# Performance work log

Hardware: AMD Instinct MI355X
Metric: run time of the kernel (lower is better)

The kernel has to match this reference:

```python
import jax, jax.numpy as jnp
import numpy as np

ATT = 256
NUM_GENES = 2128
HIDDEN = 512
B, T = 128, 1024


def setup_inputs() -> dict:
    key = jax.random.key(0)
    ks = jax.random.split(key, 8)
    return {
        "genes": jax.random.normal(ks[0], (B, NUM_GENES), dtype=jnp.float32),
        "smiles": jax.random.normal(ks[1], (B, T, HIDDEN), dtype=jnp.float32),
        "w_num_gene_features": jax.random.normal(ks[2], (1,), dtype=jnp.float32) * 0.1,
        "w_genes": jax.random.normal(ks[3], (NUM_GENES, ATT), dtype=jnp.float32) * 0.1,
        "b_genes": jax.random.normal(ks[4], (ATT,), dtype=jnp.float32) * 0.1,
        "dense_kernel": jax.random.normal(ks[5], (HIDDEN, ATT), dtype=jnp.float32) * 0.05,
        "dense_bias": jnp.zeros((ATT,), dtype=jnp.float32),
        "v": jax.random.normal(ks[6], (ATT,), dtype=jnp.float32) * 0.1,
    }


def reference(genes, smiles, w_num_gene_features, w_genes, b_genes,
              dense_kernel, dense_bias, v):
    # genes: [B, G]; collapse trivial feature axis via scalar weight -> [B, G]
    genes_collapsed = genes * w_num_gene_features[0]
    # gene context: [B, A]
    gene_proj = genes_collapsed @ w_genes + b_genes
    # smiles projection: [B, T, A]
    smiles_proj = jnp.einsum('bth,ha->bta', smiles, dense_kernel) + dense_bias
    # additive attention energies
    x = jnp.tanh(gene_proj[:, None, :] + smiles_proj)          # [B, T, A]
    xv = jnp.einsum('bta,a->bt', x, v)                          # [B, T]
    alphas = jax.nn.softmax(xv, axis=-1)                        # [B, T]
    output = jnp.einsum('bth,bt->bh', smiles, alphas)           # [B, H]
    return output, alphas
```

## Files before the change

### kernel.cpp

```cpp
#include <hip/hip_runtime.h>
#include <stdint.h>

#define B_ 128
#define T_ 1024
#define H_ 512
#define A_ 256
#define G_ 2128

typedef short s16x8 __attribute__((ext_vector_type(8)));
typedef float f32x4 __attribute__((ext_vector_type(4)));
typedef unsigned int u32;

__device__ inline unsigned short f2bf(float f) {
  unsigned u = __float_as_uint(f);
  u += 0x7fff + ((u >> 16) & 1);
  return (unsigned short)(u >> 16);
}
__device__ inline unsigned pack2bf(float a, float b) {
  return ((unsigned)f2bf(b) << 16) | f2bf(a);
}
__device__ inline float bf_lo(unsigned u) { return __uint_as_float(u << 16); }
__device__ inline float bf_hi(unsigned u) { return __uint_as_float(u & 0xffff0000u); }
__device__ inline float fast_tanh(float x) {
  x = fminf(15.f, fmaxf(-15.f, x));
  float e = __expf(2.f * x);
  return (e - 1.f) * __builtin_amdgcn_rcpf(e + 1.f);
}
__device__ inline void gl_lds16(const void* g, void* l) {
  __builtin_amdgcn_global_load_lds(
      (const __attribute__((address_space(1))) u32*)g,
      (__attribute__((address_space(3))) u32*)l, 16, 0, 0);
}

__global__ void prep_kt(const float* __restrict__ K,
                        unsigned short* __restrict__ khi) {
  int idx = blockIdx.x * 256 + threadIdx.x;
  int h = idx >> 8;
  int a = idx & 255;
  int kb = h >> 5, k = h & 31;
  int grp = k >> 3, sub = k & 7;
  khi[kb * 8192 + a * 32 + ((grp ^ (a & 3)) * 8) + sub] = f2bf(K[idx]);
}

__global__ __launch_bounds__(256) void convert_k(const float* __restrict__ smiles,
                                                 unsigned short* __restrict__ smb) {
  int f = blockIdx.x * 256 + threadIdx.x;
  int h8 = f & 63;
  int t = (f >> 6) & 1023;
  int b = f >> 16;
  const float* src = smiles + ((size_t)(b * 1024 + t)) * 512 + h8 * 8;
  float4 a0 = *reinterpret_cast<const float4*>(src);
  float4 a1 = *reinterpret_cast<const float4*>(src + 4);
  uint4 p;
  p.x = pack2bf(a0.x, a0.y); p.y = pack2bf(a0.z, a0.w);
  p.z = pack2bf(a1.x, a1.y); p.w = pack2bf(a1.z, a1.w);
  int tb = t >> 6, tp = t & 63, kb = h8 >> 2, g = h8 & 3;
  size_t dst = ((((size_t)b * 16 + tb) * 16 + kb) * 64 + tp) * 32
             + ((g ^ (tp & 3)) * 8);
  *reinterpret_cast<uint4*>(smb + dst) = p;
}

__global__ __launch_bounds__(256) void gene_proj_k(
    const float* __restrict__ genes, const float* __restrict__ w0p,
    const float* __restrict__ Wg, const float* __restrict__ bg,
    const float* __restrict__ db, float* __restrict__ gp) {
  __shared__ float sg[532];
  int b = blockIdx.x;
  int gc = blockIdx.y;
  int a = threadIdx.x;
  int g0 = gc * 532;
  for (int i = threadIdx.x; i < 532; i += 256) sg[i] = genes[(size_t)b * G_ + g0 + i];
  __syncthreads();
  float s = 0.f;
  #pragma unroll 8
  for (int g = 0; g < 532; ++g)
    s = fmaf(sg[g], Wg[(size_t)(g0 + g) * A_ + a], s);
  float val = w0p[0] * s;
  if (gc == 0) val += bg[a] + db[a];
  atomicAdd(&gp[b * A_ + a], val);
}

__global__ __launch_bounds__(256, 4) void pass1(
    const unsigned short* __restrict__ smb, const unsigned short* __restrict__ khi,
    const float* __restrict__ gp, const float* __restrict__ v,
    float* __restrict__ xv) {
  __shared__ unsigned short sA[64 * 32];
  __shared__ unsigned short sB[256 * 32];
  __shared__ float sXV[64 * 4];

  const int tid = threadIdx.x;
  const int b = blockIdx.y;
  const int tb = blockIdx.x;
  const int lane = tid & 63;
  const int w = tid >> 6;
  const int n = lane & 15;
  const int q = lane >> 4;

  const unsigned short* Ab = smb + (((size_t)b * 16 + tb) * 16) * 2048;

  f32x4 acc[4][4];
  #pragma unroll
  for (int i = 0; i < 4; ++i)
    #pragma unroll
    for (int j = 0; j < 4; ++j)
      acc[i][j] = (f32x4){0.f, 0.f, 0.f, 0.f};

  for (int kb = 0; kb < 16; ++kb) {
    __syncthreads();
    gl_lds16(Ab + kb * 2048 + w * 512 + lane * 8, &sA[w * 512]);
    #pragma unroll
    for (int r = 0; r < 4; ++r)
      gl_lds16(khi + kb * 8192 + w * 2048 + r * 512 + lane * 8,
               &sB[w * 2048 + r * 512]);
    __syncthreads();

    s16x8 af[4], bh[4];
    const int sw = (q ^ (n & 3)) * 8;
    #pragma unroll
    for (int i = 0; i < 4; ++i)
      af[i] = *reinterpret_cast<const s16x8*>(&sA[(i * 16 + n) * 32 + sw]);
    #pragma unroll
    for (int j = 0; j < 4; ++j)
      bh[j] = *reinterpret_cast<const s16x8*>(&sB[(w * 64 + j * 16 + n) * 32 + sw]);
    #pragma unroll
    for (int i = 0; i < 4; ++i)
      #pragma unroll
      for (int j = 0; j < 4; ++j)
        acc[i][j] = __builtin_amdgcn_mfma_f32_16x16x32_bf16(af[i], bh[j], acc[i][j], 0, 0, 0);
  }

  float vv[4], gg[4];
  #pragma unroll
  for (int j = 0; j < 4; ++j) {
    int a = w * 64 + j * 16 + n;
    vv[j] = v[a];
    gg[j] = gp[b * A_ + a];
  }
  #pragma unroll
  for (int i = 0; i < 4; ++i) {
    #pragma unroll
    for (int r = 0; r < 4; ++r) {
      float s = 0.f;
      #pragma unroll
      for (int j = 0; j < 4; ++j)
        s += vv[j] * fast_tanh(acc[i][j][r] + gg[j]);
      s += __shfl_xor(s, 1); s += __shfl_xor(s, 2);
      s += __shfl_xor(s, 4); s += __shfl_xor(s, 8);
      if (n == 0) sXV[(i * 16 + q * 4 + r) * 4 + w] = s;
    }
  }
  __syncthreads();
  if (tid < 64) {
    float* p = &sXV[tid * 4];
    xv[(size_t)b * T_ + tb * 64 + tid] = p[0] + p[1] + p[2] + p[3];
  }
}

__global__ __launch_bounds__(256) void softmax_k(const float* __restrict__ xv,
                                                 float* __restrict__ alphas) {
  __shared__ float red[8];
  int b = blockIdx.x, tid = threadIdx.x;
  float4 x = *reinterpret_cast<const float4*>(xv + b * T_ + tid * 4);
  float m = fmaxf(fmaxf(x.x, x.y), fmaxf(x.z, x.w));
  #pragma unroll
  for (int o = 1; o < 64; o <<= 1) m = fmaxf(m, __shfl_xor(m, o));
  if ((tid & 63) == 0) red[tid >> 6] = m;
  __syncthreads();
  m = fmaxf(fmaxf(red[0], red[1]), fmaxf(red[2], red[3]));
  float e0 = __expf(x.x - m), e1 = __expf(x.y - m);
  float e2 = __expf(x.z - m), e3 = __expf(x.w - m);
  float s = e0 + e1 + e2 + e3;
  #pragma unroll
  for (int o = 1; o < 64; o <<= 1) s += __shfl_xor(s, o);
  if ((tid & 63) == 0) red[4 + (tid >> 6)] = s;
  __syncthreads();
  s = red[4] + red[5] + red[6] + red[7];
  float inv = 1.f / s;
  float4 o4;
  o4.x = e0 * inv; o4.y = e1 * inv; o4.z = e2 * inv; o4.w = e3 * inv;
  *reinterpret_cast<float4*>(alphas + b * T_ + tid * 4) = o4;
}

__global__ __launch_bounds__(256) void pass3(const unsigned short* __restrict__ smb,
                                             const float* __restrict__ alphas,
                                             float* __restrict__ out) {
  __shared__ float red[3][64][8];
  int b = blockIdx.y, ts = blockIdx.x;
  int tid = threadIdx.x;
  int hg = tid & 63, tq = tid >> 6;
  int kb = hg >> 2, g = hg & 3;
  float acc[8] = {0.f, 0.f, 0.f, 0.f, 0.f, 0.f, 0.f, 0.f};
  for (int tb = ts * 4; tb < ts * 4 + 4; ++tb) {
    const unsigned short* tile = smb + (((size_t)b * 16 + tb) * 16 + kb) * 2048;
    const float* al = alphas + b * T_ + tb * 64;
    #pragma unroll 4
    for (int tt = 0; tt < 16; ++tt) {
      int tp = tq * 16 + tt;
      float a = al[tp];
      uint4 d = *reinterpret_cast<const uint4*>(tile + tp * 32 + ((g ^ (tp & 3)) * 8));
      acc[0] = fmaf(a, bf_lo(d.x), acc[0]); acc[1] = fmaf(a, bf_hi(d.x), acc[1]);
      acc[2] = fmaf(a, bf_lo(d.y), acc[2]); acc[3] = fmaf(a, bf_hi(d.y), acc[3]);
      acc[4] = fmaf(a, bf_lo(d.z), acc[4]); acc[5] = fmaf(a, bf_hi(d.z), acc[5]);
      acc[6] = fmaf(a, bf_lo(d.w), acc[6]); acc[7] = fmaf(a, bf_hi(d.w), acc[7]);
    }
  }
  if (tq) {
    #pragma unroll
    for (int e = 0; e < 8; ++e) red[tq - 1][hg][e] = acc[e];
  }
  __syncthreads();
  if (tq == 0) {
    float* op = out + (size_t)b * H_ + kb * 32 + g * 8;
    #pragma unroll
    for (int e = 0; e < 8; ++e)
      atomicAdd(op + e, acc[e] + red[0][hg][e] + red[1][hg][e] + red[2][hg][e]);
  }
}

extern "C" void kernel_launch(void* const* d_in, const int* in_sizes, int n_in,
                              void* d_out, int out_size, void* d_ws, size_t ws_size,
                              hipStream_t stream) {
  const float* genes  = (const float*)d_in[0];
  const float* smiles = (const float*)d_in[1];
  const float* w0     = (const float*)d_in[2];
  const float* wg     = (const float*)d_in[3];
  const float* bg     = (const float*)d_in[4];
  const float* dk     = (const float*)d_in[5];
  const float* db     = (const float*)d_in[6];
  const float* v      = (const float*)d_in[7];
  float* out = (float*)d_out;
  char* ws = (char*)d_ws;
  float* gp = (float*)ws;
  unsigned short* khi = (unsigned short*)(ws + 131072);
  float* xv = (float*)(ws + 131072 + 262144);
  unsigned short* smb = (unsigned short*)(ws + (1 << 20));
  float* alphas = out + B_ * H_;

  hipMemsetAsync(gp, 0, B_ * A_ * sizeof(float), stream);
  hipMemsetAsync(out, 0, B_ * H_ * sizeof(float), stream);
  prep_kt<<<512, 256, 0, stream>>>(dk, khi);
  convert_k<<<32768, 256, 0, stream>>>(smiles, smb);
  gene_proj_k<<<dim3(B_, 4), 256, 0, stream>>>(genes, w0, wg, bg, db, gp);
  pass1<<<dim3(16, B_), 256, 0, stream>>>(smb, khi, gp, v, xv);
  softmax_k<<<B_, 256, 0, stream>>>(xv, alphas);
  pass3<<<dim3(4, B_), 256, 0, stream>>>(smb, alphas, out);
}
```

Measured before the change: 527.2 us.

## Fuse fp32-to-bf16 smiles conversion into pass1 GEMM tile loading

Removes the separate convert_k kernel and has pass1 read fp32 smiles directly, convert each tile to bf16 in registers, write it into LDS, and also write the swizzled bf16 copy to global for pass3. The next k-block's fp32 values are prefetched into registers during the MFMA compute. This avoids one full read pass of the bf16 buffer and one kernel launch, but pass1 now issues plain global loads instead of the direct-to-LDS load path and adds register pressure.

Measured after the change: 507.3 us. 3.8% less time.

```diff
diff --git a/kernel.cpp b/kernel.cpp
--- a/kernel.cpp
+++ b/kernel.cpp
@@ -40,24 +40,6 @@
   int kb = h >> 5, k = h & 31;
   int grp = k >> 3, sub = k & 7;
   khi[kb * 8192 + a * 32 + ((grp ^ (a & 3)) * 8) + sub] = f2bf(K[idx]);
-}
-
-__global__ __launch_bounds__(256) void convert_k(const float* __restrict__ smiles,
-                                                 unsigned short* __restrict__ smb) {
-  int f = blockIdx.x * 256 + threadIdx.x;
-  int h8 = f & 63;
-  int t = (f >> 6) & 1023;
-  int b = f >> 16;
-  const float* src = smiles + ((size_t)(b * 1024 + t)) * 512 + h8 * 8;
-  float4 a0 = *reinterpret_cast<const float4*>(src);
-  float4 a1 = *reinterpret_cast<const float4*>(src + 4);
-  uint4 p;
-  p.x = pack2bf(a0.x, a0.y); p.y = pack2bf(a0.z, a0.w);
-  p.z = pack2bf(a1.x, a1.y); p.w = pack2bf(a1.z, a1.w);
-  int tb = t >> 6, tp = t & 63, kb = h8 >> 2, g = h8 & 3;
-  size_t dst = ((((size_t)b * 16 + tb) * 16 + kb) * 64 + tp) * 32
-             + ((g ^ (tp & 3)) * 8);
-  *reinterpret_cast<uint4*>(smb + dst) = p;
 }
 
 __global__ __launch_bounds__(256) void gene_proj_k(
@@ -81,9 +63,9 @@
 }
 
 __global__ __launch_bounds__(256, 4) void pass1(
-    const unsigned short* __restrict__ smb, const unsigned short* __restrict__ khi,
-    const float* __restrict__ gp, const float* __restrict__ v,
-    float* __restrict__ xv) {
+    const float* __restrict__ smiles, const unsigned short* __restrict__ khi,
+    unsigned short* __restrict__ smb, const float* __restrict__ gp,
+    const float* __restrict__ v, float* __restrict__ xv) {
   __shared__ unsigned short sA[64 * 32];
   __shared__ unsigned short sB[256 * 32];
   __shared__ float sXV[64 * 4];
@@ -96,7 +78,12 @@
   const int n = lane & 15;
   const int q = lane >> 4;
 
-  const unsigned short* Ab = smb + (((size_t)b * 16 + tb) * 16) * 2048;
+  const int ar = tid >> 2;
+  const int ac = tid & 3;
+  const int swg = (ac ^ (ar & 3)) * 8;
+  const float* asrc = smiles + ((size_t)(b * 1024 + tb * 64 + ar)) * 512 + ac * 8;
+  unsigned short* adst =
+      smb + ((((size_t)(b * 16 + tb)) * 16 * 64 + ar) * 32) + swg;
 
   f32x4 acc[4][4];
   #pragma unroll
@@ -105,14 +92,25 @@
     for (int j = 0; j < 4; ++j)
       acc[i][j] = (f32x4){0.f, 0.f, 0.f, 0.f};
 
+  float4 f0 = *reinterpret_cast<const float4*>(asrc);
+  float4 f1 = *reinterpret_cast<const float4*>(asrc + 4);
+
   for (int kb = 0; kb < 16; ++kb) {
     __syncthreads();
-    gl_lds16(Ab + kb * 2048 + w * 512 + lane * 8, &sA[w * 512]);
+    uint4 p;
+    p.x = pack2bf(f0.x, f0.y); p.y = pack2bf(f0.z, f0.w);
+    p.z = pack2bf(f1.x, f1.y); p.w = pack2bf(f1.z, f1.w);
+    *reinterpret_cast<uint4*>(&sA[ar * 32 + swg]) = p;
+    *reinterpret_cast<uint4*>(adst + kb * 2048) = p;
     #pragma unroll
     for (int r = 0; r < 4; ++r)
       gl_lds16(khi + kb * 8192 + w * 2048 + r * 512 + lane * 8,
                &sB[w * 2048 + r * 512]);
     __syncthreads();
+    if (kb < 15) {
+      f0 = *reinterpret_cast<const float4*>(asrc + (kb + 1) * 32);
+      f1 = *reinterpret_cast<const float4*>(asrc + (kb + 1) * 32 + 4);
+    }
 
     s16x8 af[4], bh[4];
     const int sw = (q ^ (n & 3)) * 8;
@@ -239,9 +237,8 @@
   hipMemsetAsync(gp, 0, B_ * A_ * sizeof(float), stream);
   hipMemsetAsync(out, 0, B_ * H_ * sizeof(float), stream);
   prep_kt<<<512, 256, 0, stream>>>(dk, khi);
-  convert_k<<<32768, 256, 0, stream>>>(smiles, smb);
   gene_proj_k<<<dim3(B_, 4), 256, 0, stream>>>(genes, w0, wg, bg, db, gp);
-  pass1<<<dim3(16, B_), 256, 0, stream>>>(smb, khi, gp, v, xv);
+  pass1<<<dim3(16, B_), 256, 0, stream>>>(smiles, khi, smb, gp, v, xv);
   softmax_k<<<B_, 256, 0, stream>>>(xv, alphas);
   pass3<<<dim3(4, B_), 256, 0, stream>>>(smb, alphas, out);
 }
```
